# Kernel optimization log

Hardware: AMD Instinct MI355X
Metric: run time of the kernel (lower is better)

Reference implementation:

```python
import jax, jax.numpy as jnp
import numpy as np

N = 8192        # num nodes
D = 512         # hidden_dim
E = 262144      # num edges (avg degree 32)
STEPS = 3       # diffusion_steps


def setup_inputs() -> dict:
    key = jax.random.key(0)
    k1, k2, k3 = jax.random.split(key, 3)
    x = jax.random.normal(k1, (N, D), dtype=jnp.float32)
    edge_index = jax.random.randint(k2, (2, E), 0, N, dtype=jnp.int32)
    W = jax.random.normal(k3, (D, D), dtype=jnp.float32) / np.sqrt(D)
    b = jnp.zeros((D,), dtype=jnp.float32)
    diffusion_weights = jnp.ones((STEPS + 1,), dtype=jnp.float32) / (STEPS + 1)
    return {"x": x, "edge_index": edge_index, "W": W, "b": b,
            "diffusion_weights": diffusion_weights}


def reference(x, edge_index, W, b, diffusion_weights):
    # linear transform
    h = x @ W + b                                   # [N, D]
    # build symmetric normalized dense adjacency (faithful to original)
    row, col = edge_index[0], edge_index[1]
    adj = jnp.zeros((N, N), dtype=h.dtype)
    adj = adj.at[row, col].set(1.0)                 # adj[row, col] = 1
    adj = adj.at[col, row].set(1.0)                 # adj[col, row] = 1
    adj = adj + jnp.eye(N, dtype=h.dtype)           # self loops
    row_sum = adj.sum(axis=1, keepdims=True)
    adj = adj / jnp.maximum(row_sum, 1.0)           # row-normalize, clamp(min=1)
    # K-hop diffusion with learned per-hop weights
    out = diffusion_weights[0] * h
    cur = h
    for i in range(STEPS):
        cur = adj @ cur                             # [N, D]
        out = out + diffusion_weights[i + 1] * cur
    # relu; dropout is identity in eval mode
    return jax.nn.relu(out)
```

## Files before the change

### kernel.cpp

```cpp
#include <hip/hip_runtime.h>
#include <hip/hip_bf16.h>

#define NN 8192
#define DD 512
#define ROWWORDS (NN / 32)
#define MAXDEG 128
#define QCHUNK 256
#define SCL 8.0f

typedef __attribute__((ext_vector_type(8))) short short8;
typedef __attribute__((ext_vector_type(4))) float floatx4;
typedef __attribute__((ext_vector_type(2))) float f32x2;

__device__ __forceinline__ unsigned short f2bf(float f) {
    union { float f; unsigned u; } v; v.f = f;
    unsigned u = v.u;
    return (unsigned short)((u + 0x7FFFu + ((u >> 16) & 1u)) >> 16);
}
__device__ __forceinline__ float bf2f(unsigned short s) {
    union { unsigned x; float f; } v; v.x = (unsigned)s << 16; return v.f;
}

__global__ __launch_bounds__(256) void prep_k(uint4* __restrict__ bm16,
                                              const float* __restrict__ x,
                                              unsigned short* __restrict__ xb,
                                              unsigned char* __restrict__ xq,
                                              const float* __restrict__ W,
                                              unsigned short* __restrict__ wbT,
                                              unsigned char* __restrict__ b1q,
                                              unsigned char* __restrict__ b2q) {
    const int j = blockIdx.x * 256 + threadIdx.x;
    bm16[j] = make_uint4(0u, 0u, 0u, 0u);
    const float4* xv = (const float4*)x;
    float4 v0 = xv[2 * j];
    float4 v1 = xv[2 * j + 1];
    ushort4 o0, o1;
    o0.x = f2bf(v0.x); o0.y = f2bf(v0.y); o0.z = f2bf(v0.z); o0.w = f2bf(v0.w);
    o1.x = f2bf(v1.x); o1.y = f2bf(v1.y); o1.z = f2bf(v1.z); o1.w = f2bf(v1.w);
    ((ushort4*)xb)[2 * j] = o0;
    ((ushort4*)xb)[2 * j + 1] = o1;
    unsigned qa = __builtin_amdgcn_cvt_pk_fp8_f32(SCL * v0.x, SCL * v0.y, 0, false);
    qa = __builtin_amdgcn_cvt_pk_fp8_f32(SCL * v0.z, SCL * v0.w, qa, true);
    unsigned qb = __builtin_amdgcn_cvt_pk_fp8_f32(SCL * v1.x, SCL * v1.y, 0, false);
    qb = __builtin_amdgcn_cvt_pk_fp8_f32(SCL * v1.z, SCL * v1.w, qb, true);
    ((uint2*)xq)[j] = make_uint2(qa, qb);
    if (j < DD * DD / 2) {
#pragma unroll
        for (int r = 0; r < 2; ++r) {
            int idx = j + r * (DD * DD / 2);
            int k = idx >> 9, c = idx & 511;
            wbT[(size_t)c * DD + k] = f2bf(W[idx]);
        }
    }
    if (blockIdx.x < 3 && threadIdx.x < 128) {
        unsigned char* pr = (blockIdx.x == 0 ? xq : blockIdx.x == 1 ? b1q : b2q)
                            + (size_t)NN * DD;
        ((unsigned*)pr)[threadIdx.x] = 0u;
    }
}

__global__ __launch_bounds__(256) void edges_k(const int* __restrict__ ei,
                                               unsigned* __restrict__ bm, int E) {
    int e = blockIdx.x * 256 + threadIdx.x;
    if (e >= E) return;
    int r = ei[e];
    int c = ei[E + e];
    atomicOr(&bm[(size_t)r * ROWWORDS + (c >> 5)], 1u << (c & 31));
    atomicOr(&bm[(size_t)c * ROWWORDS + (r >> 5)], 1u << (r & 31));
}

__global__ __launch_bounds__(256) void decode_k(const unsigned* __restrict__ bm,
                                                unsigned short* __restrict__ cols,
                                                int* __restrict__ deg) {
    const int i = blockIdx.x * 4 + (threadIdx.x >> 6);
    const int t = threadIdx.x & 63;
    const unsigned* rw = bm + (size_t)i * ROWWORDS + t * 4;
    unsigned w0 = rw[0], w1 = rw[1], w2 = rw[2], w3 = rw[3];
    int c = __popc(w0) + __popc(w1) + __popc(w2) + __popc(w3);
    int s = c;
    for (int d = 1; d < 64; d <<= 1) {
        int v = __shfl_up(s, d, 64);
        if (t >= d) s += v;
    }
    int p = s - c;
    const int n = __shfl(s, 63, 64);
    unsigned short* base = cols + (size_t)i * MAXDEG;
    const int cb = t * 128;
#pragma unroll
    for (int q = 0; q < 4; ++q) {
        unsigned w = (q == 0) ? w0 : (q == 1) ? w1 : (q == 2) ? w2 : w3;
        while (w) {
            int b = __ffs(w) - 1;
            w &= (w - 1);
            if (p < MAXDEG) base[p] = (unsigned short)(cb + q * 32 + b);
            ++p;
        }
    }
    if (t == 63) {
        int nc = (n < MAXDEG) ? n : MAXDEG;
        int npad = (nc + 15) & ~15;
        for (int q = nc; q < npad; ++q) base[q] = (unsigned short)NN;
        deg[i] = n;
    }
}

#define CVT(u, w) __builtin_amdgcn_cvt_pk_f32_fp8((int)(u), w)

#define ISSUE(P, js) do { \
    P##0 = *(const unsigned*)(cur + (size_t)(unsigned short)(js)[0] * DD + off); \
    P##1 = *(const unsigned*)(cur + (size_t)(unsigned short)(js)[1] * DD + off); \
    P##2 = *(const unsigned*)(cur + (size_t)(unsigned short)(js)[2] * DD + off); \
    P##3 = *(const unsigned*)(cur + (size_t)(unsigned short)(js)[3] * DD + off); \
    P##4 = *(const unsigned*)(cur + (size_t)(unsigned short)(js)[4] * DD + off); \
    P##5 = *(const unsigned*)(cur + (size_t)(unsigned short)(js)[5] * DD + off); \
    P##6 = *(const unsigned*)(cur + (size_t)(unsigned short)(js)[6] * DD + off); \
    P##7 = *(const unsigned*)(cur + (size_t)(unsigned short)(js)[7] * DD + off); \
} while (0)

#define CONSUME(P) do { \
    lA += CVT(P##0, false); hA += CVT(P##0, true); \
    lB += CVT(P##1, false); hB += CVT(P##1, true); \
    lA += CVT(P##2, false); hA += CVT(P##2, true); \
    lB += CVT(P##3, false); hB += CVT(P##3, true); \
    lA += CVT(P##4, false); hA += CVT(P##4, true); \
    lB += CVT(P##5, false); hB += CVT(P##5, true); \
    lA += CVT(P##6, false); hA += CVT(P##6, true); \
    lB += CVT(P##7, false); hB += CVT(P##7, true); \
} while (0)

__global__ __launch_bounds__(64) void spmm_k(const unsigned char* __restrict__ cur,
                                             unsigned char* __restrict__ nxt,
                                             const unsigned short* __restrict__ cols,
                                             const int* __restrict__ deg,
                                             const float* __restrict__ dw,
                                             const unsigned short* __restrict__ xb,
                                             const unsigned char* __restrict__ b1q,
                                             const unsigned char* __restrict__ b2q,
                                             unsigned short* __restrict__ yb,
                                             int last) {
    const int bid = blockIdx.x;
    const int chunk = bid & 1;
    const int i = bid >> 1;
    const int t = threadIdx.x;
    const int off = chunk * QCHUNK + 4 * t;
    const size_t rowb = (size_t)i * DD;
    const int n = deg[i];
    const int nc = (n < MAXDEG) ? n : MAXDEG;
    const int nb = ((nc + 15) & ~15) >> 3;
    const unsigned short* cl = cols + (size_t)i * MAXDEG;

    const unsigned eu = *(const unsigned*)(cur + rowb + off);

    f32x2 lA = {0.f, 0.f}, hA = lA, lB = lA, hB = lA;
    if (nb) {
        unsigned cA0, cA1, cA2, cA3, cA4, cA5, cA6, cA7;
        unsigned cB0, cB1, cB2, cB3, cB4, cB5, cB6, cB7;
        short8 jsA = *(const short8*)(cl);
        ISSUE(cA, jsA);
        short8 jsB = *(const short8*)(cl + 8);
        ISSUE(cB, jsB);
        for (int b = 2; b < nb; b += 2) {
            short8 jsC = *(const short8*)(cl + (size_t)b * 8);
            short8 jsD = *(const short8*)(cl + (size_t)b * 8 + 8);
            CONSUME(cA);
            ISSUE(cA, jsC);
            CONSUME(cB);
            ISSUE(cB, jsD);
        }
        CONSUME(cA);
        CONSUME(cB);
    }
    f32x2 lo = lA + lB;
    f32x2 hi = hA + hB;
    lo += CVT(eu, false);
    hi += CVT(eu, true);
    const float inv = 1.0f / (float)(n + 1);
    lo *= inv; hi *= inv;

    if (!last) {
        unsigned o = __builtin_amdgcn_cvt_pk_fp8_f32(lo.x, lo.y, 0, false);
        o = __builtin_amdgcn_cvt_pk_fp8_f32(hi.x, hi.y, o, true);
        *(unsigned*)(nxt + rowb + off) = o;
    } else {
        const float w0 = dw[0];
        const float s1 = dw[1] * (1.0f / SCL);
        const float s2 = dw[2] * (1.0f / SCL);
        const float s3 = dw[3] * (1.0f / SCL);
        ushort4 xv = *(const ushort4*)(xb + rowb + off);
        unsigned u1 = *(const unsigned*)(b1q + rowb + off);
        unsigned u2 = *(const unsigned*)(b2q + rowb + off);
        f32x2 b1l = CVT(u1, false), b1h = CVT(u1, true);
        f32x2 b2l = CVT(u2, false), b2h = CVT(u2, true);
        float y0 = w0 * bf2f(xv.x) + s1 * b1l.x + s2 * b2l.x + s3 * lo.x;
        float y1 = w0 * bf2f(xv.y) + s1 * b1l.y + s2 * b2l.y + s3 * lo.y;
        float y2 = w0 * bf2f(xv.z) + s1 * b1h.x + s2 * b2h.x + s3 * hi.x;
        float y3 = w0 * bf2f(xv.w) + s1 * b1h.y + s2 * b2h.y + s3 * hi.y;
        ushort4 o;
        o.x = f2bf(y0); o.y = f2bf(y1); o.z = f2bf(y2); o.w = f2bf(y3);
        *(ushort4*)(yb + rowb + off) = o;
    }
}

__global__ __launch_bounds__(256) void gemm_k(const unsigned short* __restrict__ yb,
                                              const unsigned short* __restrict__ wbT,
                                              const float* __restrict__ bias,
                                              const float* __restrict__ dw, int nw,
                                              float* __restrict__ out) {
    __shared__ unsigned short Asm[128][40];
    __shared__ unsigned short Bsm[128][40];
    const int t = threadIdx.x;
    const int l = t & 63;
    const int wid = t >> 6;
    const int wm = wid >> 1, wn = wid & 1;
    const int row0 = blockIdx.x * 128;
    const int col0 = blockIdx.y * 128;
    const int lr = l & 15;
    const int kk = (l >> 4) * 8;

    floatx4 acc[4][4];
#pragma unroll
    for (int a = 0; a < 4; ++a)
#pragma unroll
        for (int b = 0; b < 4; ++b) acc[a][b] = (floatx4){0.f, 0.f, 0.f, 0.f};

    for (int k0 = 0; k0 < DD; k0 += 32) {
#pragma unroll
        for (int p = 0; p < 2; ++p) {
            int e = p * 256 + t;
            int r = e >> 2;
            int kc = (e & 3) * 8;
            *(short8*)(&Asm[r][kc]) =
                *(const short8*)(yb + (size_t)(row0 + r) * DD + k0 + kc);
            *(short8*)(&Bsm[r][kc]) =
                *(const short8*)(wbT + (size_t)(col0 + r) * DD + k0 + kc);
        }
        __syncthreads();
        short8 af[4], bf[4];
#pragma unroll
        for (int mt = 0; mt < 4; ++mt)
            af[mt] = *(const short8*)(&Asm[wm * 64 + mt * 16 + lr][kk]);
#pragma unroll
        for (int nt = 0; nt < 4; ++nt)
            bf[nt] = *(const short8*)(&Bsm[wn * 64 + nt * 16 + lr][kk]);
#pragma unroll
        for (int mt = 0; mt < 4; ++mt)
#pragma unroll
            for (int nt = 0; nt < 4; ++nt)
                acc[mt][nt] = __builtin_amdgcn_mfma_f32_16x16x32_bf16(
                    af[mt], bf[nt], acc[mt][nt], 0, 0, 0);
        __syncthreads();
    }

    float sb = 0.f;
    for (int q = 0; q < nw; ++q) sb += dw[q];
#pragma unroll
    for (int nt = 0; nt < 4; ++nt) {
        int col = col0 + wn * 64 + nt * 16 + lr;
        float bv = bias[col] * sb;
#pragma unroll
        for (int mt = 0; mt < 4; ++mt) {
            int rowb = row0 + wm * 64 + mt * 16 + (l >> 4) * 4;
#pragma unroll
            for (int r = 0; r < 4; ++r) {
                float v = acc[mt][nt][r] + bv;
                v = fmaxf(v, 0.0f);
                out[(size_t)(rowb + r) * DD + col] = v;
            }
        }
    }
}

extern "C" void kernel_launch(void* const* d_in, const int* in_sizes, int n_in,
                              void* d_out, int out_size, void* d_ws, size_t ws_size,
                              hipStream_t stream) {
    const float* x    = (const float*)d_in[0];
    const int*   ei   = (const int*)d_in[1];
    const float* W    = (const float*)d_in[2];
    const float* bias = (const float*)d_in[3];
    const float* dw   = (const float*)d_in[4];
    const int E = in_sizes[1] / 2;
    const int nw = in_sizes[4];

    char* outc = (char*)d_out;
    unsigned* bitmap     = (unsigned*)outc;
    unsigned short* cols = (unsigned short*)(outc + (size_t)8 * 1024 * 1024);
    int* deg             = (int*)(outc + (size_t)12 * 1024 * 1024);

    const size_t MB = 1024 * 1024;
    char* ws = (char*)d_ws;
    unsigned short* xb  = (unsigned short*)(ws);
    unsigned short* yb  = (unsigned short*)(ws + 8 * MB);
    unsigned short* wbT = (unsigned short*)(ws + 16 * MB);
    unsigned char*  xq  = (unsigned char*)(ws + 17 * MB);
    unsigned char*  b1q = (unsigned char*)(ws + 22 * MB);
    unsigned char*  b2q = (unsigned char*)(ws + 27 * MB);

    prep_k<<<2048, 256, 0, stream>>>((uint4*)bitmap, x, xb, xq, W, wbT, b1q, b2q);
    edges_k<<<(E + 255) / 256, 256, 0, stream>>>(ei, bitmap, E);
    decode_k<<<NN / 4, 256, 0, stream>>>(bitmap, cols, deg);

    spmm_k<<<NN * 2, 64, 0, stream>>>(xq,  b1q, cols, deg, dw, xb, b1q, b2q, yb, 0);
    spmm_k<<<NN * 2, 64, 0, stream>>>(b1q, b2q, cols, deg, dw, xb, b1q, b2q, yb, 0);
    spmm_k<<<NN * 2, 64, 0, stream>>>(b2q, b1q, cols, deg, dw, xb, b1q, b2q, yb, 1);

    gemm_k<<<dim3(NN / 128, DD / 128), 256, 0, stream>>>(yb, wbT, bias, dw, nw,
                                                         (float*)d_out);
}
```

Before: 109.4 us.

## Use direct global-to-LDS loads with XOR swizzle and K=64 tiles in GEMM

The GEMM now stages A and B tiles with global_load_lds 16-byte direct copies instead of loading through registers. It uses an XOR-swizzled unpadded LDS layout to avoid bank conflicts, and doubles the K step to 64 so there are half as many barrier pairs. The SpMM kernel also gets a launch_bounds occupancy hint of 8. The risks are the correctness of the swizzle and the 16-byte LDS-load path on this target, and higher LDS use per block.

```diff
diff --git a/kernel.cpp b/kernel.cpp
--- a/kernel.cpp
+++ b/kernel.cpp
@@ -11,6 +11,8 @@
 typedef __attribute__((ext_vector_type(8))) short short8;
 typedef __attribute__((ext_vector_type(4))) float floatx4;
 typedef __attribute__((ext_vector_type(2))) float f32x2;
+typedef __attribute__((address_space(1))) const unsigned GASu;
+typedef __attribute__((address_space(3))) unsigned LASu;
 
 __device__ __forceinline__ unsigned short f2bf(float f) {
     union { float f; unsigned u; } v; v.f = f;
@@ -128,7 +130,7 @@
     lB += CVT(P##7, false); hB += CVT(P##7, true); \
 } while (0)
 
-__global__ __launch_bounds__(64) void spmm_k(const unsigned char* __restrict__ cur,
+__global__ __launch_bounds__(64, 8) void spmm_k(const unsigned char* __restrict__ cur,
                                              unsigned char* __restrict__ nxt,
                                              const unsigned short* __restrict__ cols,
                                              const int* __restrict__ deg,
@@ -206,8 +208,8 @@
                                               const float* __restrict__ bias,
                                               const float* __restrict__ dw, int nw,
                                               float* __restrict__ out) {
-    __shared__ unsigned short Asm[128][40];
-    __shared__ unsigned short Bsm[128][40];
+    __shared__ unsigned short Asm[128 * 64];
+    __shared__ unsigned short Bsm[128 * 64];
     const int t = threadIdx.x;
     const int l = t & 63;
     const int wid = t >> 6;
@@ -215,7 +217,6 @@
     const int row0 = blockIdx.x * 128;
     const int col0 = blockIdx.y * 128;
     const int lr = l & 15;
-    const int kk = (l >> 4) * 8;
 
     floatx4 acc[4][4];
 #pragma unroll
@@ -223,31 +224,43 @@
 #pragma unroll
         for (int b = 0; b < 4; ++b) acc[a][b] = (floatx4){0.f, 0.f, 0.f, 0.f};
 
-    for (int k0 = 0; k0 < DD; k0 += 32) {
-#pragma unroll
-        for (int p = 0; p < 2; ++p) {
+    for (int k0 = 0; k0 < DD; k0 += 64) {
+#pragma unroll
+        for (int p = 0; p < 4; ++p) {
             int e = p * 256 + t;
-            int r = e >> 2;
-            int kc = (e & 3) * 8;
-            *(short8*)(&Asm[r][kc]) =
-                *(const short8*)(yb + (size_t)(row0 + r) * DD + k0 + kc);
-            *(short8*)(&Bsm[r][kc]) =
-                *(const short8*)(wbT + (size_t)(col0 + r) * DD + k0 + kc);
+            int r = e >> 3;
+            int sl = e & 7;
+            int gs = (sl ^ (r & 7)) * 8;
+            __builtin_amdgcn_global_load_lds(
+                (GASu*)(yb + (size_t)(row0 + r) * DD + k0 + gs),
+                (LASu*)(Asm + (size_t)e * 8), 16, 0, 0);
+            __builtin_amdgcn_global_load_lds(
+                (GASu*)(wbT + (size_t)(col0 + r) * DD + k0 + gs),
+                (LASu*)(Bsm + (size_t)e * 8), 16, 0, 0);
         }
         __syncthreads();
-        short8 af[4], bf[4];
-#pragma unroll
-        for (int mt = 0; mt < 4; ++mt)
-            af[mt] = *(const short8*)(&Asm[wm * 64 + mt * 16 + lr][kk]);
-#pragma unroll
-        for (int nt = 0; nt < 4; ++nt)
-            bf[nt] = *(const short8*)(&Bsm[wn * 64 + nt * 16 + lr][kk]);
-#pragma unroll
-        for (int mt = 0; mt < 4; ++mt)
-#pragma unroll
-            for (int nt = 0; nt < 4; ++nt)
-                acc[mt][nt] = __builtin_amdgcn_mfma_f32_16x16x32_bf16(
-                    af[mt], bf[nt], acc[mt][nt], 0, 0, 0);
+#pragma unroll
+        for (int ks = 0; ks < 2; ++ks) {
+            short8 af[4], bf[4];
+#pragma unroll
+            for (int mt = 0; mt < 4; ++mt) {
+                int R = wm * 64 + mt * 16 + lr;
+                int sl = (l >> 4) + 4 * ks;
+                af[mt] = *(const short8*)(Asm + R * 64 + (sl ^ (R & 7)) * 8);
+            }
+#pragma unroll
+            for (int nt = 0; nt < 4; ++nt) {
+                int R = wn * 64 + nt * 16 + lr;
+                int sl = (l >> 4) + 4 * ks;
+                bf[nt] = *(const short8*)(Bsm + R * 64 + (sl ^ (R & 7)) * 8);
+            }
+#pragma unroll
+            for (int mt = 0; mt < 4; ++mt)
+#pragma unroll
+                for (int nt = 0; nt < 4; ++nt)
+                    acc[mt][nt] = __builtin_amdgcn_mfma_f32_16x16x32_bf16(
+                        af[mt], bf[nt], acc[mt][nt], 0, 0, 0);
+        }
         __syncthreads();
     }
 
```

New measurement: 104.1 us, median of 2. -4.9%, faster.
